# Kernel optimization log

Measured on AMD Instinct MI355X. Metric: run time of the kernel, lower is better.

Reference implementation:

```python
import jax, jax.numpy as jnp
import numpy as np

N = 32768      # total nodes (2048 graphs * 16 nodes)
E = 491520     # total edges (2048 graphs * 16*15)
F = 11         # in_node_nf
H = 64         # hidden_nf
G = 2048       # number of graphs
NN = 16        # nodes per graph
R = 1024       # n_reactions
L = 4          # n_layers
EIN = 2 * H + 1        # edge_mlp input: [h[row], h[col], radial]
NIN = H + H + F        # node_mlp input: [h, agg, node_attr=h0]


def setup_inputs() -> dict:
    key = jax.random.key(0)
    ks = jax.random.split(key, 24)
    s = 0.05
    d = {
        "h0": jax.random.normal(ks[0], (N, F), jnp.float32),
        "positions": jax.random.normal(ks[1], (N, 3), jnp.float32),
        "edges": jax.random.randint(ks[2], (2, E), 0, N),
        "node_mask": jnp.ones((N, 1), jnp.float32),
        "edge_mask": jnp.ones((E, 1), jnp.float32),
        "reaction_indexes": jax.random.randint(ks[3], (G,), 0, R),
        "reaction_signs": jax.random.normal(ks[4], (G,), jnp.float32),
        # params
        "emb_w": jax.random.normal(ks[5], (F, H), jnp.float32) * s,
        "emb_b": jnp.zeros((H,), jnp.float32),
        "edge_w1": jax.random.normal(ks[6], (L, EIN, H), jnp.float32) * s,
        "edge_b1": jnp.zeros((L, H), jnp.float32),
        "edge_w2": jax.random.normal(ks[7], (L, H, H), jnp.float32) * s,
        "edge_b2": jnp.zeros((L, H), jnp.float32),
        "node_w1": jax.random.normal(ks[8], (L, NIN, H), jnp.float32) * s,
        "node_b1": jnp.zeros((L, H), jnp.float32),
        "node_w2": jax.random.normal(ks[9], (L, H, H), jnp.float32) * s,
        "node_b2": jnp.zeros((L, H), jnp.float32),
        "dec_w1": jax.random.normal(ks[10], (H, H), jnp.float32) * s,
        "dec_b1": jnp.zeros((H,), jnp.float32),
        "dec_w2": jax.random.normal(ks[11], (H, H), jnp.float32) * s,
        "dec_b2": jnp.zeros((H,), jnp.float32),
        "g_w1": jax.random.normal(ks[12], (H, H), jnp.float32) * s,
        "g_b1": jnp.zeros((H,), jnp.float32),
        "g_w2": jax.random.normal(ks[13], (H, 1), jnp.float32) * s,
        "g_b2": jnp.zeros((1,), jnp.float32),
        "n_nodes": NN,
        "n_reactions": R,
    }
    return d


def reference(h0, positions, edges, node_mask, edge_mask, reaction_indexes,
              reaction_signs, emb_w, emb_b, edge_w1, edge_b1, edge_w2, edge_b2,
              node_w1, node_b1, node_w2, node_b2, dec_w1, dec_b1, dec_w2,
              dec_b2, g_w1, g_b1, g_w2, g_b2, n_nodes, n_reactions):
    silu = jax.nn.silu
    row, col = edges[0], edges[1]
    n = h0.shape[0]

    # radial is constant across layers (coords never updated in this variant)
    coord_diff = positions[row] - positions[col]          # [E, 3]
    radial = jnp.sum(coord_diff ** 2, axis=1, keepdims=True)  # [E, 1]

    h = h0 @ emb_w + emb_b                                # [N, H]
    for i in range(edge_w1.shape[0]):
        # edge model
        e_in = jnp.concatenate([h[row], h[col], radial], axis=1)  # [E, 2H+1]
        e = silu(e_in @ edge_w1[i] + edge_b1[i])
        e = silu(e @ edge_w2[i] + edge_b2[i])             # [E, H]
        e = e * edge_mask
        # scatter-sum aggregation by source node
        agg = jax.ops.segment_sum(e, row, num_segments=n)  # [N, H]
        # node model (node_attr = h0)
        n_in = jnp.concatenate([h, agg, h0], axis=1)      # [N, 2H+F]
        h = silu(n_in @ node_w1[i] + node_b1[i]) @ node_w2[i] + node_b2[i]

    # node decoder
    h = silu(h @ dec_w1 + dec_b1) @ dec_w2 + dec_b2
    h = h * node_mask
    # pool per graph (fixed n_nodes per graph)
    hg = h.reshape(-1, n_nodes, h.shape[-1]).sum(axis=1)  # [G, H]
    # graph decoder
    temp = silu(hg @ g_w1 + g_b1) @ g_w2 + g_b2           # [G, 1]
    # signed per-reaction aggregation
    pred = jnp.zeros((n_reactions,), h.dtype).at[reaction_indexes].add(
        temp[:, 0] * reaction_signs)
    return pred
```

## Files before the change

kernel.cpp:

```cpp
#include <hip/hip_runtime.h>
#include <math.h>
#include <stdint.h>

#define N_NODES 32768
#define N_EDGES 491520
#define F_IN    11
#define H       64
#define G_GRAPHS 2048
#define NN_PER_G 16
#define R_REACT 1024
#define L_LAYERS 4
#define EIN     129
#define NIN     139
#define NPBLK   32

#define WPROJ 0
#define WE2   65536
#define WN1   98304
#define WN2   180224
#define WD1   212992
#define WD2   221184
#define WEMB  229376
#define WTOT  233472

typedef __attribute__((ext_vector_type(8))) short short8;
typedef __attribute__((ext_vector_type(4))) float f32x4;

__device__ __forceinline__ float silu_f(float x) {
    return x * __builtin_amdgcn_rcpf(1.0f + __expf(-x));
}
__device__ __forceinline__ void atomAddF(float* p, float v) {
    unsafeAtomicAdd(p, v);
}
__device__ __forceinline__ float bf2f(unsigned short b) {
    union { float f; unsigned u; } v; v.u = ((unsigned)b) << 16;
    return v.f;
}
__device__ __forceinline__ unsigned short f2bf(float x) {
    union { float f; unsigned u; } v; v.f = x;
    unsigned r = v.u + 0x7FFFu + ((v.u >> 16) & 1u);
    return (unsigned short)(r >> 16);
}
__device__ __forceinline__ void splitbf(float x, unsigned short& hi, unsigned short& lo) {
    hi = f2bf(x);
    lo = f2bf(x - bf2f(hi));
}
__device__ __forceinline__ void splitbf_t(float x, unsigned short& hi, unsigned short& lo) {
    union { float f; unsigned u; } v; v.f = x;
    hi = (unsigned short)(v.u >> 16);
    union { float f; unsigned u; } w; w.f = x - bf2f(hi);
    lo = (unsigned short)(w.u >> 16);
}

__global__ __launch_bounds__(64) void k_prepw(
        const float* __restrict__ ew1, const float* __restrict__ ew2,
        const float* __restrict__ nw1, const float* __restrict__ nw2,
        const float* __restrict__ dw1, const float* __restrict__ dw2,
        const float* __restrict__ embw,
        short* __restrict__ wsW) {
    const int b = blockIdx.x;
    const int lane = threadIdx.x;
    const int quad = lane >> 4, m16 = lane & 15;
    short8 h8, l8;
    short* base; int fidx, half;

    if (b < 64) {
        int l = b >> 4, f = b & 15;
        int nt = f >> 1, kf = f & 1;
#pragma unroll
        for (int j = 0; j < 8; ++j) {
            int row = (nt >= 4 ? 64 : 0) + kf * 32 + quad * 8 + j;
            unsigned short hi, lo;
            splitbf(ew1[l * EIN * H + row * H + (nt & 3) * 16 + m16], hi, lo);
            h8[j] = (short)hi; l8[j] = (short)lo;
        }
        base = wsW + WPROJ + l * 16384; fidx = f; half = 8192;
    } else if (b < 96) {
        int bb = b - 64; int l = bb >> 3, f = bb & 7;
        int nt = f >> 1, kf = f & 1;
#pragma unroll
        for (int j = 0; j < 8; ++j) {
            int row = kf * 32 + quad * 8 + j;
            unsigned short hi, lo;
            splitbf(ew2[l * H * H + row * H + nt * 16 + m16], hi, lo);
            h8[j] = (short)hi; l8[j] = (short)lo;
        }
        base = wsW + WE2 + l * 8192; fidx = f; half = 4096;
    } else if (b < 176) {
        int bb = b - 96; int l = bb / 20, f = bb % 20;
        int nt = f / 5, kf = f % 5;
#pragma unroll
        for (int j = 0; j < 8; ++j) {
            int row = kf * 32 + quad * 8 + j;
            float w = (row < NIN) ? nw1[l * NIN * H + row * H + nt * 16 + m16] : 0.0f;
            unsigned short hi, lo; splitbf(w, hi, lo);
            h8[j] = (short)hi; l8[j] = (short)lo;
        }
        base = wsW + WN1 + l * 20480; fidx = f; half = 10240;
    } else if (b < 208) {
        int bb = b - 176; int l = bb >> 3, f = bb & 7;
        int nt = f >> 1, kf = f & 1;
#pragma unroll
        for (int j = 0; j < 8; ++j) {
            int row = kf * 32 + quad * 8 + j;
            unsigned short hi, lo;
            splitbf(nw2[l * H * H + row * H + nt * 16 + m16], hi, lo);
            h8[j] = (short)hi; l8[j] = (short)lo;
        }
        base = wsW + WN2 + l * 8192; fidx = f; half = 4096;
    } else if (b < 216) {
        int f = b - 208;
        int nt = f >> 1, kf = f & 1;
#pragma unroll
        for (int j = 0; j < 8; ++j) {
            int row = kf * 32 + quad * 8 + j;
            unsigned short hi, lo;
            splitbf(dw1[row * H + nt * 16 + m16], hi, lo);
            h8[j] = (short)hi; l8[j] = (short)lo;
        }
        base = wsW + WD1; fidx = f; half = 4096;
    } else if (b < 224) {
        int f = b - 216;
        int nt = f >> 1, kf = f & 1;
#pragma unroll
        for (int j = 0; j < 8; ++j) {
            int row = kf * 32 + quad * 8 + j;
            unsigned short hi, lo;
            splitbf(dw2[row * H + nt * 16 + m16], hi, lo);
            h8[j] = (short)hi; l8[j] = (short)lo;
        }
        base = wsW + WD2; fidx = f; half = 4096;
    } else {
        int f = b - 224;
#pragma unroll
        for (int j = 0; j < 8; ++j) {
            int row = quad * 8 + j;
            float w = (row < F_IN) ? embw[row * H + f * 16 + m16] : 0.0f;
            unsigned short hi, lo; splitbf(w, hi, lo);
            h8[j] = (short)hi; l8[j] = (short)lo;
        }
        base = wsW + WEMB; fidx = f; half = 2048;
    }
    *(short8*)(base + (fidx * 64 + lane) * 8) = h8;
    *(short8*)(base + half + (fidx * 64 + lane) * 8) = l8;
}

__global__ __launch_bounds__(256) void k_hist(
        const int* __restrict__ edges, int* __restrict__ deg) {
    int e = blockIdx.x * 256 + threadIdx.x;
    atomicAdd(&deg[edges[e]], 1);
}

__global__ __launch_bounds__(128) void k_scan_blk(
        const int* __restrict__ deg, int* __restrict__ off,
        int* __restrict__ bsum) {
    __shared__ int sd[128];
    int b = blockIdx.x;
    sd[threadIdx.x] = deg[b * 128 + threadIdx.x];
    __syncthreads();
    if (threadIdx.x == 0) {
        int s = 0;
        for (int i = 0; i < 128; ++i) { int d = sd[i]; sd[i] = s; s += d; }
        bsum[b] = s;
    }
    __syncthreads();
    off[b * 128 + threadIdx.x] = sd[threadIdx.x];
}

__global__ __launch_bounds__(256) void k_scan_top(
        const int* __restrict__ bsum, int* __restrict__ bbase) {
    __shared__ int sb[256];
    sb[threadIdx.x] = bsum[threadIdx.x];
    __syncthreads();
    if (threadIdx.x == 0) {
        int s = 0;
        for (int i = 0; i < 256; ++i) { int d = sb[i]; sb[i] = s; s += d; }
    }
    __syncthreads();
    bbase[threadIdx.x] = sb[threadIdx.x];
}

__global__ __launch_bounds__(256) void k_cursor(
        const int* __restrict__ off, const int* __restrict__ bbase,
        int* __restrict__ nstart, int* __restrict__ cursor) {
    int n = blockIdx.x * 256 + threadIdx.x;
    int ns = off[n] + bbase[n >> 7];
    nstart[n] = ns;
    cursor[n] = ns;
    if (n == 0) nstart[N_NODES] = N_EDGES;
}

__global__ __launch_bounds__(256) void k_fill(
        const int* __restrict__ edges, const float* __restrict__ posi,
        const float* __restrict__ emask, int* __restrict__ cursor,
        float4* __restrict__ csrQ) {
    int e = blockIdx.x * 256 + threadIdx.x;
    int r = edges[e], c = edges[N_EDGES + e];
    float dx = posi[r * 3 + 0] - posi[c * 3 + 0];
    float dy = posi[r * 3 + 1] - posi[c * 3 + 1];
    float dz = posi[r * 3 + 2] - posi[c * 3 + 2];
    float rad = dx * dx + dy * dy + dz * dz;
    int p = atomicAdd(&cursor[r], 1);
    int pk = c | ((r & (NPBLK - 1)) << 16);
    csrQ[p] = make_float4(__int_as_float(pk), rad, emask[e], 0.0f);
}

__global__ __launch_bounds__(64, 2) void k_embed_proj(
        const float* __restrict__ h0, const short* __restrict__ wEmb,
        const float* __restrict__ emb_b,
        const short* __restrict__ wP, const float* __restrict__ eb1,
        float* __restrict__ h, float* __restrict__ PA, float* __restrict__ PB) {
    const int lane = threadIdx.x;
    const int quad = lane >> 4, m16 = lane & 15;
    const int nb = blockIdx.x * 16;
    __shared__ float tld[16 * 68];

    float a0[8];
    const float* h0p = h0 + (nb + m16) * F_IN;
#pragma unroll
    for (int j = 0; j < 8; ++j) {
        int kk = quad * 8 + j;
        a0[j] = (kk < F_IN) ? h0p[kk] : 0.0f;
    }
    short8 A0h, A0l;
#pragma unroll
    for (int j = 0; j < 8; ++j) {
        unsigned short hi, lo; splitbf_t(a0[j], hi, lo);
        A0h[j] = (short)hi; A0l[j] = (short)lo;
    }
    float ebv[4];
#pragma unroll
    for (int nt = 0; nt < 4; ++nt) ebv[nt] = emb_b[nt * 16 + m16];

#pragma unroll
    for (int nt = 0; nt < 4; ++nt) {
        short8 bh = *(const short8*)(wEmb + (nt * 64 + lane) * 8);
        short8 bl = *(const short8*)(wEmb + 2048 + (nt * 64 + lane) * 8);
        f32x4 a = {0.0f, 0.0f, 0.0f, 0.0f};
        a = __builtin_amdgcn_mfma_f32_16x16x32_bf16(A0h, bh, a, 0, 0, 0);
        a = __builtin_amdgcn_mfma_f32_16x16x32_bf16(A0h, bl, a, 0, 0, 0);
        a = __builtin_amdgcn_mfma_f32_16x16x32_bf16(A0l, bh, a, 0, 0, 0);
#pragma unroll
        for (int r4 = 0; r4 < 4; ++r4) {
            const int node = nb + quad * 4 + r4;
            float hv = a[r4] + ebv[nt];
            h[node * H + nt * 16 + m16] = hv;
            tld[(quad * 4 + r4) * 68 + nt * 16 + m16] = hv;
        }
    }
    __syncthreads();
    float av[16];
    *(float4*)&av[0]  = *(const float4*)&tld[m16 * 68 + quad * 8 + 0];
    *(float4*)&av[4]  = *(const float4*)&tld[m16 * 68 + quad * 8 + 4];
    *(float4*)&av[8]  = *(const float4*)&tld[m16 * 68 + quad * 8 + 32];
    *(float4*)&av[12] = *(const float4*)&tld[m16 * 68 + quad * 8 + 36];
    short8 Ah0, Ah1, Al0, Al1;
#pragma unroll
    for (int j = 0; j < 8; ++j) {
        unsigned short hi, lo;
        splitbf_t(av[j], hi, lo);     Ah0[j] = (short)hi; Al0[j] = (short)lo;
        splitbf_t(av[8 + j], hi, lo); Ah1[j] = (short)hi; Al1[j] = (short)lo;
    }
    float b1v[4];
#pragma unroll
    for (int nt = 0; nt < 4; ++nt) b1v[nt] = eb1[nt * 16 + m16];
#pragma unroll
    for (int nt = 0; nt < 8; ++nt) {
        short8 bh0 = *(const short8*)(wP + ((nt*2+0) * 64 + lane) * 8);
        short8 bh1 = *(const short8*)(wP + ((nt*2+1) * 64 + lane) * 8);
        short8 bl0 = *(const short8*)(wP + 8192 + ((nt*2+0) * 64 + lane) * 8);
        short8 bl1 = *(const short8*)(wP + 8192 + ((nt*2+1) * 64 + lane) * 8);
        f32x4 a = {0.0f, 0.0f, 0.0f, 0.0f};
        a = __builtin_amdgcn_mfma_f32_16x16x32_bf16(Ah0, bh0, a, 0, 0, 0);
        a = __builtin_amdgcn_mfma_f32_16x16x32_bf16(Ah1, bh1, a, 0, 0, 0);
        a = __builtin_amdgcn_mfma_f32_16x16x32_bf16(Ah0, bl0, a, 0, 0, 0);
        a = __builtin_amdgcn_mfma_f32_16x16x32_bf16(Ah1, bl1, a, 0, 0, 0);
        a = __builtin_amdgcn_mfma_f32_16x16x32_bf16(Al0, bh0, a, 0, 0, 0);
        a = __builtin_amdgcn_mfma_f32_16x16x32_bf16(Al1, bh1, a, 0, 0, 0);
#pragma unroll
        for (int r4 = 0; r4 < 4; ++r4) {
            const int node = nb + quad * 4 + r4;
            if (nt < 4)
                PA[node * H + nt * 16 + m16] = a[r4] + b1v[nt];
            else
                PB[node * H + (nt - 4) * 16 + m16] = a[r4];
        }
    }
}

__global__ __launch_bounds__(256, 3) void k_edge6(
        const float* __restrict__ PA, const float* __restrict__ PB,
        const int* __restrict__ nstart, const float4* __restrict__ csrQ,
        const float* __restrict__ W1,
        const short* __restrict__ wE2, const float* __restrict__ b2,
        float* __restrict__ agg) {
    const int tid = threadIdx.x;
    const int lane = tid & 63, wave = tid >> 6;
    const int quad = lane >> 4, m16 = lane & 15;
    const int n0 = blockIdx.x * NPBLK;

    __shared__ float aggld[NPBLK * 68];
    for (int i = tid; i < NPBLK * 68; i += 256) aggld[i] = 0.0f;

    short8 Bh[8], Bl[8];
#pragma unroll
    for (int f = 0; f < 8; ++f) {
        Bh[f] = *(const short8*)(wE2 + (f * 64 + lane) * 8);
        Bl[f] = *(const short8*)(wE2 + 4096 + (f * 64 + lane) * 8);
    }
    float w1cr[16];
#pragma unroll
    for (int i = 0; i < 16; ++i) {
        int k = (i < 8) ? (quad * 8 + i) : (32 + quad * 8 + (i - 8));
        w1cr[i] = W1[128 * H + k];
    }
    float b2v[4];
#pragma unroll
    for (int nt = 0; nt < 4; ++nt) b2v[nt] = b2[nt * 16 + m16];

    const int start = nstart[n0];
    const int end   = nstart[n0 + NPBLK];
    __syncthreads();

    const int ntiles = (end - start + 15) >> 4;

    int   pkA = 0, pkB = 0;
    float radA = 0.0f, radB = 0.0f;
    float avA[16], bvA[16];

    int tA = wave;
    bool haveA = tA < ntiles;
    if (haveA) {
        const int idx = start + tA * 16 + m16;
        const int ss  = min(idx, N_EDGES - 1);
        float4 q = csrQ[ss];
        pkA  = __float_as_int(q.x);
        radA = q.y;
        const int c  = pkA & 0xFFFF;
        const int rl = pkA >> 16;
        const float* par = PA + (n0 + rl) * H + quad * 8;
        const float* pbr = PB + c * H + quad * 8;
        *(float4*)&avA[0]  = *(const float4*)(par + 0);
        *(float4*)&avA[4]  = *(const float4*)(par + 4);
        *(float4*)&avA[8]  = *(const float4*)(par + 32);
        *(float4*)&avA[12] = *(const float4*)(par + 36);
        *(float4*)&bvA[0]  = *(const float4*)(pbr + 0);
        *(float4*)&bvA[4]  = *(const float4*)(pbr + 4);
        *(float4*)&bvA[8]  = *(const float4*)(pbr + 32);
        *(float4*)&bvA[12] = *(const float4*)(pbr + 36);
    }
    int tB = tA + 4;
    bool haveB = tB < ntiles;
    if (haveB) {
        const int idx = start + tB * 16 + m16;
        const int ss  = min(idx, N_EDGES - 1);
        float4 q = csrQ[ss];
        pkB  = __float_as_int(q.x);
        radB = q.y;
    }

    while (haveA) {
        float bvB[16];
        if (haveB) {
            const int c = pkB & 0xFFFF;
            const float* pbr = PB + c * H + quad * 8;
            *(float4*)&bvB[0]  = *(const float4*)(pbr + 0);
            *(float4*)&bvB[4]  = *(const float4*)(pbr + 4);
            *(float4*)&bvB[8]  = *(const float4*)(pbr + 32);
            *(float4*)&bvB[12] = *(const float4*)(pbr + 36);
        }
        const int tC = tB + 4;
        const bool haveC = tC < ntiles;
        int pkC = 0; float radC = 0.0f;
        if (haveC) {
            const int idx = start + tC * 16 + m16;
            const int ss  = min(idx, N_EDGES - 1);
            float4 q = csrQ[ss];
            pkC  = __float_as_int(q.x);
            radC = q.y;
        }
        int rlq[4]; float mkq[4];
        const int sb = start + tA * 16 + quad * 4;
#pragma unroll
        for (int r4 = 0; r4 < 4; ++r4) {
            int s = sb + r4, s2 = min(s, N_EDGES - 1);
            float4 q = csrQ[s2];
            rlq[r4] = __float_as_int(q.x) >> 16;
            mkq[r4] = (s < end) ? q.z : 0.0f;
        }

        short8 Ah0, Ah1, Al0, Al1;
#pragma unroll
        for (int i = 0; i < 8; ++i) {
            unsigned short hi, lo;
            splitbf_t(silu_f(avA[i] + bvA[i] + radA * w1cr[i]), hi, lo);
            Ah0[i] = (short)hi; Al0[i] = (short)lo;
            splitbf_t(silu_f(avA[8+i] + bvA[8+i] + radA * w1cr[8+i]), hi, lo);
            Ah1[i] = (short)hi; Al1[i] = (short)lo;
        }
        f32x4 acc[4];
#pragma unroll
        for (int nt = 0; nt < 4; ++nt) {
            f32x4 a = {0.0f, 0.0f, 0.0f, 0.0f};
            a = __builtin_amdgcn_mfma_f32_16x16x32_bf16(Ah0, Bh[nt*2+0], a, 0, 0, 0);
            a = __builtin_amdgcn_mfma_f32_16x16x32_bf16(Ah1, Bh[nt*2+1], a, 0, 0, 0);
            a = __builtin_amdgcn_mfma_f32_16x16x32_bf16(Ah0, Bl[nt*2+0], a, 0, 0, 0);
            a = __builtin_amdgcn_mfma_f32_16x16x32_bf16(Ah1, Bl[nt*2+1], a, 0, 0, 0);
            a = __builtin_amdgcn_mfma_f32_16x16x32_bf16(Al0, Bh[nt*2+0], a, 0, 0, 0);
            a = __builtin_amdgcn_mfma_f32_16x16x32_bf16(Al1, Bh[nt*2+1], a, 0, 0, 0);
            acc[nt] = a;
        }

#pragma unroll
        for (int nt = 0; nt < 4; ++nt) {
            float oo[4];
#pragma unroll
            for (int r4 = 0; r4 < 4; ++r4)
                oo[r4] = silu_f(acc[nt][r4] + b2v[nt]) * mkq[r4];
            int cur = rlq[0]; float s = oo[0];
#pragma unroll
            for (int r4 = 1; r4 < 4; ++r4) {
                if (rlq[r4] == cur) { s += oo[r4]; }
                else {
                    atomicAdd(&aggld[cur * 68 + nt * 16 + m16], s);
                    cur = rlq[r4]; s = oo[r4];
                }
            }
            atomicAdd(&aggld[cur * 68 + nt * 16 + m16], s);
        }

        if (haveB) {
            const int rl = pkB >> 16;
            const float* par = PA + (n0 + rl) * H + quad * 8;
            *(float4*)&avA[0]  = *(const float4*)(par + 0);
            *(float4*)&avA[4]  = *(const float4*)(par + 4);
            *(float4*)&avA[8]  = *(const float4*)(par + 32);
            *(float4*)&avA[12] = *(const float4*)(par + 36);
#pragma unroll
            for (int i = 0; i < 16; ++i) bvA[i] = bvB[i];
            pkA = pkB; radA = radB;
        }
        pkB = pkC; radB = radC;
        tA = tB; tB = tC; haveA = haveB; haveB = haveC;
    }

    __syncthreads();
#pragma unroll
    for (int i = tid; i < NPBLK * 16; i += 256) {
        int n = i >> 4, cb = (i & 15) << 2;
        *(float4*)&agg[(n0 + n) * H + cb] = *(const float4*)&aggld[n * 68 + cb];
    }
}

__global__ __launch_bounds__(64, 2) void k_node_proj(
        float* __restrict__ h, const float* __restrict__ agg,
        const float* __restrict__ h0,
        const short* __restrict__ wN1, const float* __restrict__ b1,
        const short* __restrict__ wN2, const float* __restrict__ b2,
        const short* __restrict__ wPn, const float* __restrict__ eb1n,
        float* __restrict__ PA, float* __restrict__ PB) {
    const int lane = threadIdx.x;
    const int quad = lane >> 4, m16 = lane & 15;
    const int nb = blockIdx.x * 16;

    float b1v[4], b2v[4];
#pragma unroll
    for (int nt = 0; nt < 4; ++nt) {
        b1v[nt] = b1[nt * 16 + m16];
        b2v[nt] = b2[nt * 16 + m16];
    }
    __shared__ float tld[16 * 68];

    float a1[5][8];
    const float* hp = h + (nb + m16) * H + quad * 8;
    const float* ap = agg + (nb + m16) * H + quad * 8;
    *(float4*)&a1[0][0] = *(const float4*)(hp + 0);
    *(float4*)&a1[0][4] = *(const float4*)(hp + 4);
    *(float4*)&a1[1][0] = *(const float4*)(hp + 32);
    *(float4*)&a1[1][4] = *(const float4*)(hp + 36);
    *(float4*)&a1[2][0] = *(const float4*)(ap + 0);
    *(float4*)&a1[2][4] = *(const float4*)(ap + 4);
    *(float4*)&a1[3][0] = *(const float4*)(ap + 32);
    *(float4*)&a1[3][4] = *(const float4*)(ap + 36);
    const float* h0p = h0 + (nb + m16) * F_IN;
#pragma unroll
    for (int j = 0; j < 8; ++j) {
        int kk = quad * 8 + j;
        a1[4][j] = (kk < F_IN) ? h0p[kk] : 0.0f;
    }
    short8 A1h[5], A1l[5];
#pragma unroll
    for (int kf = 0; kf < 5; ++kf) {
        short8 ah, al;
#pragma unroll
        for (int j = 0; j < 8; ++j) {
            unsigned short hi, lo; splitbf_t(a1[kf][j], hi, lo);
            ah[j] = (short)hi; al[j] = (short)lo;
        }
        A1h[kf] = ah; A1l[kf] = al;
    }
#pragma unroll
    for (int nt = 0; nt < 4; ++nt) {
        short8 bh[5], bl[5];
#pragma unroll
        for (int kf = 0; kf < 5; ++kf) {
            bh[kf] = *(const short8*)(wN1 + ((nt*5+kf) * 64 + lane) * 8);
            bl[kf] = *(const short8*)(wN1 + 10240 + ((nt*5+kf) * 64 + lane) * 8);
        }
        f32x4 a = {0.0f, 0.0f, 0.0f, 0.0f};
#pragma unroll
        for (int kf = 0; kf < 5; ++kf)
            a = __builtin_amdgcn_mfma_f32_16x16x32_bf16(A1h[kf], bh[kf], a, 0, 0, 0);
#pragma unroll
        for (int kf = 0; kf < 5; ++kf)
            a = __builtin_amdgcn_mfma_f32_16x16x32_bf16(A1h[kf], bl[kf], a, 0, 0, 0);
#pragma unroll
        for (int kf = 0; kf < 5; ++kf)
            a = __builtin_amdgcn_mfma_f32_16x16x32_bf16(A1l[kf], bh[kf], a, 0, 0, 0);
#pragma unroll
        for (int r4 = 0; r4 < 4; ++r4)
            tld[(quad * 4 + r4) * 68 + nt * 16 + m16] = silu_f(a[r4] + b1v[nt]);
    }
    __syncthreads();
    float a2[16];
    *(float4*)&a2[0]  = *(const float4*)&tld[m16 * 68 + quad * 8 + 0];
    *(float4*)&a2[4]  = *(const float4*)&tld[m16 * 68 + quad * 8 + 4];
    *(float4*)&a2[8]  = *(const float4*)&tld[m16 * 68 + quad * 8 + 32];
    *(float4*)&a2[12] = *(const float4*)&tld[m16 * 68 + quad * 8 + 36];
    short8 A2h0, A2h1, A2l0, A2l1;
#pragma unroll
    for (int j = 0; j < 8; ++j) {
        unsigned short hi, lo;
        splitbf_t(a2[j], hi, lo);     A2h0[j] = (short)hi; A2l0[j] = (short)lo;
        splitbf_t(a2[8+j], hi, lo);   A2h1[j] = (short)hi; A2l1[j] = (short)lo;
    }
    __syncthreads();
#pragma unroll
    for (int nt = 0; nt < 4; ++nt) {
        short8 bh0 = *(const short8*)(wN2 + ((nt*2+0) * 64 + lane) * 8);
        short8 bh1 = *(const short8*)(wN2 + ((nt*2+1) * 64 + lane) * 8);
        short8 bl0 = *(const short8*)(wN2 + 4096 + ((nt*2+0) * 64 + lane) * 8);
        short8 bl1 = *(const short8*)(wN2 + 4096 + ((nt*2+1) * 64 + lane) * 8);
        f32x4 a = {0.0f, 0.0f, 0.0f, 0.0f};
        a = __builtin_amdgcn_mfma_f32_16x16x32_bf16(A2h0, bh0, a, 0, 0, 0);
        a = __builtin_amdgcn_mfma_f32_16x16x32_bf16(A2h1, bh1, a, 0, 0, 0);
        a = __builtin_amdgcn_mfma_f32_16x16x32_bf16(A2h0, bl0, a, 0, 0, 0);
        a = __builtin_amdgcn_mfma_f32_16x16x32_bf16(A2h1, bl1, a, 0, 0, 0);
        a = __builtin_amdgcn_mfma_f32_16x16x32_bf16(A2l0, bh0, a, 0, 0, 0);
        a = __builtin_amdgcn_mfma_f32_16x16x32_bf16(A2l1, bh1, a, 0, 0, 0);
#pragma unroll
        for (int r4 = 0; r4 < 4; ++r4) {
            const int node = nb + quad * 4 + r4;
            float hv = a[r4] + b2v[nt];
            h[node * H + nt * 16 + m16] = hv;
            tld[(quad * 4 + r4) * 68 + nt * 16 + m16] = hv;
        }
    }
    __syncthreads();
    float av[16];
    *(float4*)&av[0]  = *(const float4*)&tld[m16 * 68 + quad * 8 + 0];
    *(float4*)&av[4]  = *(const float4*)&tld[m16 * 68 + quad * 8 + 4];
    *(float4*)&av[8]  = *(const float4*)&tld[m16 * 68 + quad * 8 + 32];
    *(float4*)&av[12] = *(const float4*)&tld[m16 * 68 + quad * 8 + 36];
    short8 Ph0, Ph1, Pl0, Pl1;
#pragma unroll
    for (int j = 0; j < 8; ++j) {
        unsigned short hi, lo;
        splitbf_t(av[j], hi, lo);     Ph0[j] = (short)hi; Pl0[j] = (short)lo;
        splitbf_t(av[8+j], hi, lo);   Ph1[j] = (short)hi; Pl1[j] = (short)lo;
    }
    float b1ev[4];
#pragma unroll
    for (int nt = 0; nt < 4; ++nt) b1ev[nt] = eb1n[nt * 16 + m16];
#pragma unroll
    for (int nt = 0; nt < 8; ++nt) {
        short8 bh0 = *(const short8*)(wPn + ((nt*2+0) * 64 + lane) * 8);
        short8 bh1 = *(const short8*)(wPn + ((nt*2+1) * 64 + lane) * 8);
        short8 bl0 = *(const short8*)(wPn + 8192 + ((nt*2+0) * 64 + lane) * 8);
        short8 bl1 = *(const short8*)(wPn + 8192 + ((nt*2+1) * 64 + lane) * 8);
        f32x4 a = {0.0f, 0.0f, 0.0f, 0.0f};
        a = __builtin_amdgcn_mfma_f32_16x16x32_bf16(Ph0, bh0, a, 0, 0, 0);
        a = __builtin_amdgcn_mfma_f32_16x16x32_bf16(Ph1, bh1, a, 0, 0, 0);
        a = __builtin_amdgcn_mfma_f32_16x16x32_bf16(Ph0, bl0, a, 0, 0, 0);
        a = __builtin_amdgcn_mfma_f32_16x16x32_bf16(Ph1, bl1, a, 0, 0, 0);
        a = __builtin_amdgcn_mfma_f32_16x16x32_bf16(Pl0, bh0, a, 0, 0, 0);
        a = __builtin_amdgcn_mfma_f32_16x16x32_bf16(Pl1, bh1, a, 0, 0, 0);
#pragma unroll
        for (int r4 = 0; r4 < 4; ++r4) {
            const int node = nb + quad * 4 + r4;
            if (nt < 4)
                PA[node * H + nt * 16 + m16] = a[r4] + b1ev[nt];
            else
                PB[node * H + (nt - 4) * 16 + m16] = a[r4];
        }
    }
}

__global__ __launch_bounds__(64, 2) void k_node_dec_graph(
        const float* __restrict__ h, const float* __restrict__ agg,
        const float* __restrict__ h0,
        const short* __restrict__ wN1, const float* __restrict__ b1,
        const short* __restrict__ wN2, const float* __restrict__ b2,
        const short* __restrict__ wD1, const float* __restrict__ db1,
        const short* __restrict__ wD2, const float* __restrict__ db2,
        const float* __restrict__ nmask,
        const float* __restrict__ gW1, const float* __restrict__ gb1,
        const float* __restrict__ gW2, const float* __restrict__ gb2,
        const int* __restrict__ rid, const float* __restrict__ rsign,
        float* __restrict__ pred) {
    const int lane = threadIdx.x;
    const int quad = lane >> 4, m16 = lane & 15;
    const int nb = blockIdx.x * 16;

    float b1v[4], b2v[4], db1v[4], db2v[4];
#pragma unroll
    for (int nt = 0; nt < 4; ++nt) {
        b1v[nt]  = b1[nt * 16 + m16];
        b2v[nt]  = b2[nt * 16 + m16];
        db1v[nt] = db1[nt * 16 + m16];
        db2v[nt] = db2[nt * 16 + m16];
    }
    float nm[4];
#pragma unroll
    for (int r4 = 0; r4 < 4; ++r4) nm[r4] = nmask[nb + quad * 4 + r4];

    __shared__ float tld[16 * 68];
    __shared__ __align__(16) float hgs[64];

    float a1[5][8];
    const float* hp = h + (nb + m16) * H + quad * 8;
    const float* ap = agg + (nb + m16) * H + quad * 8;
    *(float4*)&a1[0][0] = *(const float4*)(hp + 0);
    *(float4*)&a1[0][4] = *(const float4*)(hp + 4);
    *(float4*)&a1[1][0] = *(const float4*)(hp + 32);
    *(float4*)&a1[1][4] = *(const float4*)(hp + 36);
    *(float4*)&a1[2][0] = *(const float4*)(ap + 0);
    *(float4*)&a1[2][4] = *(const float4*)(ap + 4);
    *(float4*)&a1[3][0] = *(const float4*)(ap + 32);
    *(float4*)&a1[3][4] = *(const float4*)(ap + 36);
    const float* h0p = h0 + (nb + m16) * F_IN;
#pragma unroll
    for (int j = 0; j < 8; ++j) {
        int kk = quad * 8 + j;
        a1[4][j] = (kk < F_IN) ? h0p[kk] : 0.0f;
    }
    short8 A1h[5], A1l[5];
#pragma unroll
    for (int kf = 0; kf < 5; ++kf) {
        short8 ah, al;
#pragma unroll
        for (int j = 0; j < 8; ++j) {
            unsigned short hi, lo; splitbf_t(a1[kf][j], hi, lo);
            ah[j] = (short)hi; al[j] = (short)lo;
        }
        A1h[kf] = ah; A1l[kf] = al;
    }
#pragma unroll
    for (int nt = 0; nt < 4; ++nt) {
        short8 bh[5], bl[5];
#pragma unroll
        for (int kf = 0; kf < 5; ++kf) {
            bh[kf] = *(const short8*)(wN1 + ((nt*5+kf) * 64 + lane) * 8);
            bl[kf] = *(const short8*)(wN1 + 10240 + ((nt*5+kf) * 64 + lane) * 8);
        }
        f32x4 a = {0.0f, 0.0f, 0.0f, 0.0f};
#pragma unroll
        for (int kf = 0; kf < 5; ++kf)
            a = __builtin_amdgcn_mfma_f32_16x16x32_bf16(A1h[kf], bh[kf], a, 0, 0, 0);
#pragma unroll
        for (int kf = 0; kf < 5; ++kf)
            a = __builtin_amdgcn_mfma_f32_16x16x32_bf16(A1h[kf], bl[kf], a, 0, 0, 0);
#pragma unroll
        for (int kf = 0; kf < 5; ++kf)
            a = __builtin_amdgcn_mfma_f32_16x16x32_bf16(A1l[kf], bh[kf], a, 0, 0, 0);
#pragma unroll
        for (int r4 = 0; r4 < 4; ++r4)
            tld[(quad * 4 + r4) * 68 + nt * 16 + m16] = silu_f(a[r4] + b1v[nt]);
    }
    __syncthreads();
    float a2[16];
    *(float4*)&a2[0]  = *(const float4*)&tld[m16 * 68 + quad * 8 + 0];
    *(float4*)&a2[4]  = *(const float4*)&tld[m16 * 68 + quad * 8 + 4];
    *(float4*)&a2[8]  = *(const float4*)&tld[m16 * 68 + quad * 8 + 32];
    *(float4*)&a2[12] = *(const float4*)&tld[m16 * 68 + quad * 8 + 36];
    short8 A2h0, A2h1, A2l0, A2l1;
#pragma unroll
    for (int j = 0; j < 8; ++j) {
        unsigned short hi, lo;
        splitbf_t(a2[j], hi, lo);     A2h0[j] = (short)hi; A2l0[j] = (short)lo;
        splitbf_t(a2[8+j], hi, lo);   A2h1[j] = (short)hi; A2l1[j] = (short)lo;
    }
    __syncthreads();
#pragma unroll
    for (int nt = 0; nt < 4; ++nt) {
        short8 bh0 = *(const short8*)(wN2 + ((nt*2+0) * 64 + lane) * 8);
        short8 bh1 = *(const short8*)(wN2 + ((nt*2+1) * 64 + lane) * 8);
        short8 bl0 = *(const short8*)(wN2 + 4096 + ((nt*2+0) * 64 + lane) * 8);
        short8 bl1 = *(const short8*)(wN2 + 4096 + ((nt*2+1) * 64 + lane) * 8);
        f32x4 a = {0.0f, 0.0f, 0.0f, 0.0f};
        a = __builtin_amdgcn_mfma_f32_16x16x32_bf16(A2h0, bh0, a, 0, 0, 0);
        a = __builtin_amdgcn_mfma_f32_16x16x32_bf16(A2h1, bh1, a, 0, 0, 0);
        a = __builtin_amdgcn_mfma_f32_16x16x32_bf16(A2h0, bl0, a, 0, 0, 0);
        a = __builtin_amdgcn_mfma_f32_16x16x32_bf16(A2h1, bl1, a, 0, 0, 0);
        a = __builtin_amdgcn_mfma_f32_16x16x32_bf16(A2l0, bh0, a, 0, 0, 0);
        a = __builtin_amdgcn_mfma_f32_16x16x32_bf16(A2l1, bh1, a, 0, 0, 0);
#pragma unroll
        for (int r4 = 0; r4 < 4; ++r4)
            tld[(quad * 4 + r4) * 68 + nt * 16 + m16] = a[r4] + b2v[nt];
    }
    __syncthreads();
    float av[16];
    *(float4*)&av[0]  = *(const float4*)&tld[m16 * 68 + quad * 8 + 0];
    *(float4*)&av[4]  = *(const float4*)&tld[m16 * 68 + quad * 8 + 4];
    *(float4*)&av[8]  = *(const float4*)&tld[m16 * 68 + quad * 8 + 32];
    *(float4*)&av[12] = *(const float4*)&tld[m16 * 68 + quad * 8 + 36];
    short8 Dh0, Dh1, Dl0, Dl1;
#pragma unroll
    for (int j = 0; j < 8; ++j) {
        unsigned short hi, lo;
        splitbf_t(av[j], hi, lo);     Dh0[j] = (short)hi; Dl0[j] = (short)lo;
        splitbf_t(av[8+j], hi, lo);   Dh1[j] = (short)hi; Dl1[j] = (short)lo;
    }
    __syncthreads();
#pragma unroll
    for (int nt = 0; nt < 4; ++nt) {
        short8 bh0 = *(const short8*)(wD1 + ((nt*2+0) * 64 + lane) * 8);
        short8 bh1 = *(const short8*)(wD1 + ((nt*2+1) * 64 + lane) * 8);
        short8 bl0 = *(const short8*)(wD1 + 4096 + ((nt*2+0) * 64 + lane) * 8);
        short8 bl1 = *(const short8*)(wD1 + 4096 + ((nt*2+1) * 64 + lane) * 8);
        f32x4 a = {0.0f, 0.0f, 0.0f, 0.0f};
        a = __builtin_amdgcn_mfma_f32_16x16x32_bf16(Dh0, bh0, a, 0, 0, 0);
        a = __builtin_amdgcn_mfma_f32_16x16x32_bf16(Dh1, bh1, a, 0, 0, 0);
        a = __builtin_amdgcn_mfma_f32_16x16x32_bf16(Dh0, bl0, a, 0, 0, 0);
        a = __builtin_amdgcn_mfma_f32_16x16x32_bf16(Dh1, bl1, a, 0, 0, 0);
        a = __builtin_amdgcn_mfma_f32_16x16x32_bf16(Dl0, bh0, a, 0, 0, 0);
        a = __builtin_amdgcn_mfma_f32_16x16x32_bf16(Dl1, bh1, a, 0, 0, 0);
#pragma unroll
        for (int r4 = 0; r4 < 4; ++r4)
            tld[(quad * 4 + r4) * 68 + nt * 16 + m16] = silu_f(a[r4] + db1v[nt]);
    }
    __syncthreads();
    float a3[16];
    *(float4*)&a3[0]  = *(const float4*)&tld[m16 * 68 + quad * 8 + 0];
    *(float4*)&a3[4]  = *(const float4*)&tld[m16 * 68 + quad * 8 + 4];
    *(float4*)&a3[8]  = *(const float4*)&tld[m16 * 68 + quad * 8 + 32];
    *(float4*)&a3[12] = *(const float4*)&tld[m16 * 68 + quad * 8 + 36];
    short8 Eh0, Eh1, El0, El1;
#pragma unroll
    for (int j = 0; j < 8; ++j) {
        unsigned short hi, lo;
        splitbf_t(a3[j], hi, lo);     Eh0[j] = (short)hi; El0[j] = (short)lo;
        splitbf_t(a3[8+j], hi, lo);   Eh1[j] = (short)hi; El1[j] = (short)lo;
    }
#pragma unroll
    for (int nt = 0; nt < 4; ++nt) {
        short8 bh0 = *(const short8*)(wD2 + ((nt*2+0) * 64 + lane) * 8);
        short8 bh1 = *(const short8*)(wD2 + ((nt*2+1) * 64 + lane) * 8);
        short8 bl0 = *(const short8*)(wD2 + 4096 + ((nt*2+0) * 64 + lane) * 8);
        short8 bl1 = *(const short8*)(wD2 + 4096 + ((nt*2+1) * 64 + lane) * 8);
        f32x4 a = {0.0f, 0.0f, 0.0f, 0.0f};
        a = __builtin_amdgcn_mfma_f32_16x16x32_bf16(Eh0, bh0, a, 0, 0, 0);
        a = __builtin_amdgcn_mfma_f32_16x16x32_bf16(Eh1, bh1, a, 0, 0, 0);
        a = __builtin_amdgcn_mfma_f32_16x16x32_bf16(Eh0, bl0, a, 0, 0, 0);
        a = __builtin_amdgcn_mfma_f32_16x16x32_bf16(Eh1, bl1, a, 0, 0, 0);
        a = __builtin_amdgcn_mfma_f32_16x16x32_bf16(El0, bh0, a, 0, 0, 0);
        a = __builtin_amdgcn_mfma_f32_16x16x32_bf16(El1, bh1, a, 0, 0, 0);
        float s = 0.0f;
#pragma unroll
        for (int r4 = 0; r4 < 4; ++r4)
            s += (a[r4] + db2v[nt]) * nm[r4];
        s += __shfl_xor(s, 16);
        s += __shfl_xor(s, 32);
        if (quad == 0) hgs[nt * 16 + m16] = s;
    }
    __syncthreads();
    float acc = gb1[lane];
#pragma unroll
    for (int k = 0; k < H; ++k)
        acc += hgs[k] * gW1[k * H + lane];
    float part = silu_f(acc) * gW2[lane];
#pragma unroll
    for (int off = 32; off > 0; off >>= 1)
        part += __shfl_down(part, off);
    if (lane == 0)
        atomAddF(&pred[rid[blockIdx.x]], (part + gb2[0]) * rsign[blockIdx.x]);
}

extern "C" void kernel_launch(void* const* d_in, const int* in_sizes, int n_in,
                              void* d_out, int out_size, void* d_ws, size_t ws_size,
                              hipStream_t stream) {
    const float* h0      = (const float*)d_in[0];
    const float* pos     = (const float*)d_in[1];
    const int*   edges   = (const int*)d_in[2];
    const float* nmask   = (const float*)d_in[3];
    const float* emask   = (const float*)d_in[4];
    const int*   rid     = (const int*)d_in[5];
    const float* rsign   = (const float*)d_in[6];
    const float* emb_w   = (const float*)d_in[7];
    const float* emb_b   = (const float*)d_in[8];
    const float* edge_w1 = (const float*)d_in[9];
    const float* edge_b1 = (const float*)d_in[10];
    const float* edge_w2 = (const float*)d_in[11];
    const float* edge_b2 = (const float*)d_in[12];
    const float* node_w1 = (const float*)d_in[13];
    const float* node_b1 = (const float*)d_in[14];
    const float* node_w2 = (const float*)d_in[15];
    const float* node_b2 = (const float*)d_in[16];
    const float* dec_w1  = (const float*)d_in[17];
    const float* dec_b1  = (const float*)d_in[18];
    const float* dec_w2  = (const float*)d_in[19];
    const float* dec_b2  = (const float*)d_in[20];
    const float* g_w1    = (const float*)d_in[21];
    const float* g_b1    = (const float*)d_in[22];
    const float* g_w2    = (const float*)d_in[23];
    const float* g_b2    = (const float*)d_in[24];

    float* h      = (float*)d_ws;
    float* agg    = h + N_NODES * H;
    float* PA     = agg + N_NODES * H;
    float* PB     = PA + N_NODES * H;
    float4* csrQ  = (float4*)(PB + N_NODES * H);
    int*   deg    = (int*)(csrQ + N_EDGES);
    int*   off    = deg + N_NODES;
    int*   bsum   = off + N_NODES;
    int*   bbase  = bsum + 256;
    int*   nstart = bbase + 256;
    int*   cursor = nstart + N_NODES + 1;
    short* wsW    = (short*)((((uintptr_t)(cursor + N_NODES)) + 255) & ~(uintptr_t)255);
    float* pred   = (float*)d_out;

    hipMemsetAsync(d_out, 0, R_REACT * sizeof(float), stream);
    hipMemsetAsync(deg, 0, N_NODES * sizeof(int), stream);

    k_prepw<<<228, 64, 0, stream>>>(edge_w1, edge_w2, node_w1, node_w2,
                                    dec_w1, dec_w2, emb_w, wsW);
    k_hist<<<N_EDGES / 256, 256, 0, stream>>>(edges, deg);
    k_scan_blk<<<256, 128, 0, stream>>>(deg, off, bsum);
    k_scan_top<<<1, 256, 0, stream>>>(bsum, bbase);
    k_cursor<<<N_NODES / 256, 256, 0, stream>>>(off, bbase, nstart, cursor);
    k_fill<<<N_EDGES / 256, 256, 0, stream>>>(edges, pos, emask, cursor, csrQ);
    k_embed_proj<<<N_NODES / 16, 64, 0, stream>>>(
        h0, wsW + WEMB, emb_b, wsW + WPROJ, edge_b1, h, PA, PB);

    for (int i = 0; i < L_LAYERS; ++i) {
        k_edge6<<<N_NODES / NPBLK, 256, 0, stream>>>(
            PA, PB, nstart, csrQ,
            edge_w1 + i * EIN * H,
            wsW + WE2 + i * 8192, edge_b2 + i * H, agg);
        if (i < L_LAYERS - 1) {
            k_node_proj<<<N_NODES / 16, 64, 0, stream>>>(
                h, agg, h0,
                wsW + WN1 + i * 20480, node_b1 + i * H,
                wsW + WN2 + i * 8192,  node_b2 + i * H,
                wsW + WPROJ + (i + 1) * 16384, edge_b1 + (i + 1) * H,
                PA, PB);
        } else {
            k_node_dec_graph<<<N_NODES / 16, 64, 0, stream>>>(
                h, agg, h0,
                wsW + WN1 + i * 20480, node_b1 + i * H,
                wsW + WN2 + i * 8192,  node_b2 + i * H,
                wsW + WD1, dec_b1, wsW + WD2, dec_b2,
                nmask, g_w1, g_b1, g_w2, g_b2, rid, rsign, pred);
        }
    }
}
```

Baseline: 485.7 us.

## Fuse edge aggregation with node MLP into one kernel per layer

Merges the per-layer edge kernel and the node-update/projection kernel into a single kernel, so aggregated messages stay in shared memory instead of going through a global agg buffer. PB is double-buffered so blocks can write the next layer's projection while other blocks still read the current one. Waves 2-3 duplicate the node MLP work for their half (only waves 0-1 store), and launch bounds drop to 2 blocks per CU, which can reduce occupancy for the gather-heavy edge phase.

```diff
diff --git a/kernel.cpp b/kernel.cpp
--- a/kernel.cpp
+++ b/kernel.cpp
@@ -288,200 +288,192 @@
     }
 }
 
-__global__ __launch_bounds__(256, 3) void k_edge6(
-        const float* __restrict__ PA, const float* __restrict__ PB,
+__global__ __launch_bounds__(256, 2) void k_edge_node(
+        float* __restrict__ PA, const float* __restrict__ PBin,
         const int* __restrict__ nstart, const float4* __restrict__ csrQ,
         const float* __restrict__ W1,
-        const short* __restrict__ wE2, const float* __restrict__ b2,
-        float* __restrict__ agg) {
+        const short* __restrict__ wE2, const float* __restrict__ eb2,
+        float* __restrict__ h, const float* __restrict__ h0,
+        const short* __restrict__ wN1, const float* __restrict__ nb1,
+        const short* __restrict__ wN2, const float* __restrict__ nb2,
+        const short* __restrict__ wPn, const float* __restrict__ eb1n,
+        float* __restrict__ PBout) {
     const int tid = threadIdx.x;
     const int lane = tid & 63, wave = tid >> 6;
     const int quad = lane >> 4, m16 = lane & 15;
     const int n0 = blockIdx.x * NPBLK;
 
     __shared__ float aggld[NPBLK * 68];
+    __shared__ float tld[2][16 * 68];
     for (int i = tid; i < NPBLK * 68; i += 256) aggld[i] = 0.0f;
 
-    short8 Bh[8], Bl[8];
-#pragma unroll
-    for (int f = 0; f < 8; ++f) {
-        Bh[f] = *(const short8*)(wE2 + (f * 64 + lane) * 8);
-        Bl[f] = *(const short8*)(wE2 + 4096 + (f * 64 + lane) * 8);
-    }
-    float w1cr[16];
-#pragma unroll
-    for (int i = 0; i < 16; ++i) {
-        int k = (i < 8) ? (quad * 8 + i) : (32 + quad * 8 + (i - 8));
-        w1cr[i] = W1[128 * H + k];
-    }
-    float b2v[4];
-#pragma unroll
-    for (int nt = 0; nt < 4; ++nt) b2v[nt] = b2[nt * 16 + m16];
-
-    const int start = nstart[n0];
-    const int end   = nstart[n0 + NPBLK];
-    __syncthreads();
-
-    const int ntiles = (end - start + 15) >> 4;
-
-    int   pkA = 0, pkB = 0;
-    float radA = 0.0f, radB = 0.0f;
-    float avA[16], bvA[16];
-
-    int tA = wave;
-    bool haveA = tA < ntiles;
-    if (haveA) {
-        const int idx = start + tA * 16 + m16;
-        const int ss  = min(idx, N_EDGES - 1);
-        float4 q = csrQ[ss];
-        pkA  = __float_as_int(q.x);
-        radA = q.y;
-        const int c  = pkA & 0xFFFF;
-        const int rl = pkA >> 16;
-        const float* par = PA + (n0 + rl) * H + quad * 8;
-        const float* pbr = PB + c * H + quad * 8;
-        *(float4*)&avA[0]  = *(const float4*)(par + 0);
-        *(float4*)&avA[4]  = *(const float4*)(par + 4);
-        *(float4*)&avA[8]  = *(const float4*)(par + 32);
-        *(float4*)&avA[12] = *(const float4*)(par + 36);
-        *(float4*)&bvA[0]  = *(const float4*)(pbr + 0);
-        *(float4*)&bvA[4]  = *(const float4*)(pbr + 4);
-        *(float4*)&bvA[8]  = *(const float4*)(pbr + 32);
-        *(float4*)&bvA[12] = *(const float4*)(pbr + 36);
-    }
-    int tB = tA + 4;
-    bool haveB = tB < ntiles;
-    if (haveB) {
-        const int idx = start + tB * 16 + m16;
-        const int ss  = min(idx, N_EDGES - 1);
-        float4 q = csrQ[ss];
-        pkB  = __float_as_int(q.x);
-        radB = q.y;
-    }
-
-    while (haveA) {
-        float bvB[16];
-        if (haveB) {
-            const int c = pkB & 0xFFFF;
-            const float* pbr = PB + c * H + quad * 8;
-            *(float4*)&bvB[0]  = *(const float4*)(pbr + 0);
-            *(float4*)&bvB[4]  = *(const float4*)(pbr + 4);
-            *(float4*)&bvB[8]  = *(const float4*)(pbr + 32);
-            *(float4*)&bvB[12] = *(const float4*)(pbr + 36);
-        }
-        const int tC = tB + 4;
-        const bool haveC = tC < ntiles;
-        int pkC = 0; float radC = 0.0f;
-        if (haveC) {
-            const int idx = start + tC * 16 + m16;
+    {
+        short8 Bh[8], Bl[8];
+#pragma unroll
+        for (int f = 0; f < 8; ++f) {
+            Bh[f] = *(const short8*)(wE2 + (f * 64 + lane) * 8);
+            Bl[f] = *(const short8*)(wE2 + 4096 + (f * 64 + lane) * 8);
+        }
+        float w1cr[16];
+#pragma unroll
+        for (int i = 0; i < 16; ++i) {
+            int k = (i < 8) ? (quad * 8 + i) : (32 + quad * 8 + (i - 8));
+            w1cr[i] = W1[128 * H + k];
+        }
+        float b2v[4];
+#pragma unroll
+        for (int nt = 0; nt < 4; ++nt) b2v[nt] = eb2[nt * 16 + m16];
+
+        const int start = nstart[n0];
+        const int end   = nstart[n0 + NPBLK];
+        __syncthreads();
+
+        const int ntiles = (end - start + 15) >> 4;
+
+        int   pkA = 0, pkB = 0;
+        float radA = 0.0f, radB = 0.0f;
+        float avA[16], bvA[16];
+
+        int tA = wave;
+        bool haveA = tA < ntiles;
+        if (haveA) {
+            const int idx = start + tA * 16 + m16;
             const int ss  = min(idx, N_EDGES - 1);
             float4 q = csrQ[ss];
-            pkC  = __float_as_int(q.x);
-            radC = q.y;
-        }
-        int rlq[4]; float mkq[4];
-        const int sb = start + tA * 16 + quad * 4;
-#pragma unroll
-        for (int r4 = 0; r4 < 4; ++r4) {
-            int s = sb + r4, s2 = min(s, N_EDGES - 1);
-            float4 q = csrQ[s2];
-            rlq[r4] = __float_as_int(q.x) >> 16;
-            mkq[r4] = (s < end) ? q.z : 0.0f;
-        }
-
-        short8 Ah0, Ah1, Al0, Al1;
-#pragma unroll
-        for (int i = 0; i < 8; ++i) {
-            unsigned short hi, lo;
-            splitbf_t(silu_f(avA[i] + bvA[i] + radA * w1cr[i]), hi, lo);
-            Ah0[i] = (short)hi; Al0[i] = (short)lo;
-            splitbf_t(silu_f(avA[8+i] + bvA[8+i] + radA * w1cr[8+i]), hi, lo);
-            Ah1[i] = (short)hi; Al1[i] = (short)lo;
-        }
-        f32x4 acc[4];
-#pragma unroll
-        for (int nt = 0; nt < 4; ++nt) {
-            f32x4 a = {0.0f, 0.0f, 0.0f, 0.0f};
-            a = __builtin_amdgcn_mfma_f32_16x16x32_bf16(Ah0, Bh[nt*2+0], a, 0, 0, 0);
-            a = __builtin_amdgcn_mfma_f32_16x16x32_bf16(Ah1, Bh[nt*2+1], a, 0, 0, 0);
-            a = __builtin_amdgcn_mfma_f32_16x16x32_bf16(Ah0, Bl[nt*2+0], a, 0, 0, 0);
-            a = __builtin_amdgcn_mfma_f32_16x16x32_bf16(Ah1, Bl[nt*2+1], a, 0, 0, 0);
-            a = __builtin_amdgcn_mfma_f32_16x16x32_bf16(Al0, Bh[nt*2+0], a, 0, 0, 0);
-            a = __builtin_amdgcn_mfma_f32_16x16x32_bf16(Al1, Bh[nt*2+1], a, 0, 0, 0);
-            acc[nt] = a;
-        }
-
-#pragma unroll
-        for (int nt = 0; nt < 4; ++nt) {
-            float oo[4];
-#pragma unroll
-            for (int r4 = 0; r4 < 4; ++r4)
-                oo[r4] = silu_f(acc[nt][r4] + b2v[nt]) * mkq[r4];
-            int cur = rlq[0]; float s = oo[0];
-#pragma unroll
-            for (int r4 = 1; r4 < 4; ++r4) {
-                if (rlq[r4] == cur) { s += oo[r4]; }
-                else {
-                    atomicAdd(&aggld[cur * 68 + nt * 16 + m16], s);
-                    cur = rlq[r4]; s = oo[r4];
-                }
-            }
-            atomicAdd(&aggld[cur * 68 + nt * 16 + m16], s);
-        }
-
-        if (haveB) {
-            const int rl = pkB >> 16;
+            pkA  = __float_as_int(q.x);
+            radA = q.y;
+            const int c  = pkA & 0xFFFF;
+            const int rl = pkA >> 16;
             const float* par = PA + (n0 + rl) * H + quad * 8;
+            const float* pbr = PBin + c * H + quad * 8;
             *(float4*)&avA[0]  = *(const float4*)(par + 0);
             *(float4*)&avA[4]  = *(const float4*)(par + 4);
             *(float4*)&avA[8]  = *(const float4*)(par + 32);
             *(float4*)&avA[12] = *(const float4*)(par + 36);
-#pragma unroll
-            for (int i = 0; i < 16; ++i) bvA[i] = bvB[i];
-            pkA = pkB; radA = radB;
-        }
-        pkB = pkC; radB = radC;
-        tA = tB; tB = tC; haveA = haveB; haveB = haveC;
-    }
-
-    __syncthreads();
-#pragma unroll
-    for (int i = tid; i < NPBLK * 16; i += 256) {
-        int n = i >> 4, cb = (i & 15) << 2;
-        *(float4*)&agg[(n0 + n) * H + cb] = *(const float4*)&aggld[n * 68 + cb];
-    }
-}
-
-__global__ __launch_bounds__(64, 2) void k_node_proj(
-        float* __restrict__ h, const float* __restrict__ agg,
-        const float* __restrict__ h0,
-        const short* __restrict__ wN1, const float* __restrict__ b1,
-        const short* __restrict__ wN2, const float* __restrict__ b2,
-        const short* __restrict__ wPn, const float* __restrict__ eb1n,
-        float* __restrict__ PA, float* __restrict__ PB) {
-    const int lane = threadIdx.x;
-    const int quad = lane >> 4, m16 = lane & 15;
-    const int nb = blockIdx.x * 16;
+            *(float4*)&bvA[0]  = *(const float4*)(pbr + 0);
+            *(float4*)&bvA[4]  = *(const float4*)(pbr + 4);
+            *(float4*)&bvA[8]  = *(const float4*)(pbr + 32);
+            *(float4*)&bvA[12] = *(const float4*)(pbr + 36);
+        }
+        int tB = tA + 4;
+        bool haveB = tB < ntiles;
+        if (haveB) {
+            const int idx = start + tB * 16 + m16;
+            const int ss  = min(idx, N_EDGES - 1);
+            float4 q = csrQ[ss];
+            pkB  = __float_as_int(q.x);
+            radB = q.y;
+        }
+
+        while (haveA) {
+            float bvB[16];
+            if (haveB) {
+                const int c = pkB & 0xFFFF;
+                const float* pbr = PBin + c * H + quad * 8;
+                *(float4*)&bvB[0]  = *(const float4*)(pbr + 0);
+                *(float4*)&bvB[4]  = *(const float4*)(pbr + 4);
+                *(float4*)&bvB[8]  = *(const float4*)(pbr + 32);
+                *(float4*)&bvB[12] = *(const float4*)(pbr + 36);
+            }
+            const int tC = tB + 4;
+            const bool haveC = tC < ntiles;
+            int pkC = 0; float radC = 0.0f;
+            if (haveC) {
+                const int idx = start + tC * 16 + m16;
+                const int ss  = min(idx, N_EDGES - 1);
+                float4 q = csrQ[ss];
+                pkC  = __float_as_int(q.x);
+                radC = q.y;
+            }
+            int rlq[4]; float mkq[4];
+            const int sb = start + tA * 16 + quad * 4;
+#pragma unroll
+            for (int r4 = 0; r4 < 4; ++r4) {
+                int s = sb + r4, s2 = min(s, N_EDGES - 1);
+                float4 q = csrQ[s2];
+                rlq[r4] = __float_as_int(q.x) >> 16;
+                mkq[r4] = (s < end) ? q.z : 0.0f;
+            }
+
+            short8 Ah0, Ah1, Al0, Al1;
+#pragma unroll
+            for (int i = 0; i < 8; ++i) {
+                unsigned short hi, lo;
+                splitbf_t(silu_f(avA[i] + bvA[i] + radA * w1cr[i]), hi, lo);
+                Ah0[i] = (short)hi; Al0[i] = (short)lo;
+                splitbf_t(silu_f(avA[8+i] + bvA[8+i] + radA * w1cr[8+i]), hi, lo);
+                Ah1[i] = (short)hi; Al1[i] = (short)lo;
+            }
+            f32x4 acc[4];
+#pragma unroll
+            for (int nt = 0; nt < 4; ++nt) {
+                f32x4 a = {0.0f, 0.0f, 0.0f, 0.0f};
+                a = __builtin_amdgcn_mfma_f32_16x16x32_bf16(Ah0, Bh[nt*2+0], a, 0, 0, 0);
+                a = __builtin_amdgcn_mfma_f32_16x16x32_bf16(Ah1, Bh[nt*2+1], a, 0, 0, 0);
+                a = __builtin_amdgcn_mfma_f32_16x16x32_bf16(Ah0, Bl[nt*2+0], a, 0, 0, 0);
+                a = __builtin_amdgcn_mfma_f32_16x16x32_bf16(Ah1, Bl[nt*2+1], a, 0, 0, 0);
+                a = __builtin_amdgcn_mfma_f32_16x16x32_bf16(Al0, Bh[nt*2+0], a, 0, 0, 0);
+                a = __builtin_amdgcn_mfma_f32_16x16x32_bf16(Al1, Bh[nt*2+1], a, 0, 0, 0);
+                acc[nt] = a;
+            }
+
+#pragma unroll
+            for (int nt = 0; nt < 4; ++nt) {
+                float oo[4];
+#pragma unroll
+                for (int r4 = 0; r4 < 4; ++r4)
+                    oo[r4] = silu_f(acc[nt][r4] + b2v[nt]) * mkq[r4];
+                int cur = rlq[0]; float s = oo[0];
+#pragma unroll
+                for (int r4 = 1; r4 < 4; ++r4) {
+                    if (rlq[r4] == cur) { s += oo[r4]; }
+                    else {
+                        atomicAdd(&aggld[cur * 68 + nt * 16 + m16], s);
+                        cur = rlq[r4]; s = oo[r4];
+                    }
+                }
+                atomicAdd(&aggld[cur * 68 + nt * 16 + m16], s);
+            }
+
+            if (haveB) {
+                const int rl = pkB >> 16;
+                const float* par = PA + (n0 + rl) * H + quad * 8;
+                *(float4*)&avA[0]  = *(const float4*)(par + 0);
+                *(float4*)&avA[4]  = *(const float4*)(par + 4);
+                *(float4*)&avA[8]  = *(const float4*)(par + 32);
+                *(float4*)&avA[12] = *(const float4*)(par + 36);
+#pragma unroll
+                for (int i = 0; i < 16; ++i) bvA[i] = bvB[i];
+                pkA = pkB; radA = radB;
+            }
+            pkB = pkC; radB = radC;
+            tA = tB; tB = tC; haveA = haveB; haveB = haveC;
+        }
+    }
+    __syncthreads();
+
+    const int t  = wave & 1;
+    const int nb = n0 + t * 16;
+    const bool wmain = (wave < 2);
 
     float b1v[4], b2v[4];
 #pragma unroll
     for (int nt = 0; nt < 4; ++nt) {
-        b1v[nt] = b1[nt * 16 + m16];
-        b2v[nt] = b2[nt * 16 + m16];
-    }
-    __shared__ float tld[16 * 68];
+        b1v[nt] = nb1[nt * 16 + m16];
+        b2v[nt] = nb2[nt * 16 + m16];
+    }
 
     float a1[5][8];
     const float* hp = h + (nb + m16) * H + quad * 8;
-    const float* ap = agg + (nb + m16) * H + quad * 8;
+    const float* ag = &aggld[(t * 16 + m16) * 68 + quad * 8];
     *(float4*)&a1[0][0] = *(const float4*)(hp + 0);
     *(float4*)&a1[0][4] = *(const float4*)(hp + 4);
     *(float4*)&a1[1][0] = *(const float4*)(hp + 32);
     *(float4*)&a1[1][4] = *(const float4*)(hp + 36);
-    *(float4*)&a1[2][0] = *(const float4*)(ap + 0);
-    *(float4*)&a1[2][4] = *(const float4*)(ap + 4);
-    *(float4*)&a1[3][0] = *(const float4*)(ap + 32);
-    *(float4*)&a1[3][4] = *(const float4*)(ap + 36);
+    *(float4*)&a1[2][0] = *(const float4*)(ag + 0);
+    *(float4*)&a1[2][4] = *(const float4*)(ag + 4);
+    *(float4*)&a1[3][0] = *(const float4*)(ag + 32);
+    *(float4*)&a1[3][4] = *(const float4*)(ag + 36);
     const float* h0p = h0 + (nb + m16) * F_IN;
 #pragma unroll
     for (int j = 0; j < 8; ++j) {
@@ -519,14 +511,14 @@
             a = __builtin_amdgcn_mfma_f32_16x16x32_bf16(A1l[kf], bh[kf], a, 0, 0, 0);
 #pragma unroll
         for (int r4 = 0; r4 < 4; ++r4)
-            tld[(quad * 4 + r4) * 68 + nt * 16 + m16] = silu_f(a[r4] + b1v[nt]);
+            tld[t][(quad * 4 + r4) * 68 + nt * 16 + m16] = silu_f(a[r4] + b1v[nt]);
     }
     __syncthreads();
     float a2[16];
-    *(float4*)&a2[0]  = *(const float4*)&tld[m16 * 68 + quad * 8 + 0];
-    *(float4*)&a2[4]  = *(const float4*)&tld[m16 * 68 + quad * 8 + 4];
-    *(float4*)&a2[8]  = *(const float4*)&tld[m16 * 68 + quad * 8 + 32];
-    *(float4*)&a2[12] = *(const float4*)&tld[m16 * 68 + quad * 8 + 36];
+    *(float4*)&a2[0]  = *(const float4*)&tld[t][m16 * 68 + quad * 8 + 0];
+    *(float4*)&a2[4]  = *(const float4*)&tld[t][m16 * 68 + quad * 8 + 4];
+    *(float4*)&a2[8]  = *(const float4*)&tld[t][m16 * 68 + quad * 8 + 32];
+    *(float4*)&a2[12] = *(const float4*)&tld[t][m16 * 68 + quad * 8 + 36];
     short8 A2h0, A2h1, A2l0, A2l1;
 #pragma unroll
     for (int j = 0; j < 8; ++j) {
@@ -552,16 +544,16 @@
         for (int r4 = 0; r4 < 4; ++r4) {
             const int node = nb + quad * 4 + r4;
             float hv = a[r4] + b2v[nt];
-            h[node * H + nt * 16 + m16] = hv;
-            tld[(quad * 4 + r4) * 68 + nt * 16 + m16] = hv;
+            if (wmain) h[node * H + nt * 16 + m16] = hv;
+            tld[t][(quad * 4 + r4) * 68 + nt * 16 + m16] = hv;
         }
     }
     __syncthreads();
     float av[16];
-    *(float4*)&av[0]  = *(const float4*)&tld[m16 * 68 + quad * 8 + 0];
-    *(float4*)&av[4]  = *(const float4*)&tld[m16 * 68 + quad * 8 + 4];
-    *(float4*)&av[8]  = *(const float4*)&tld[m16 * 68 + quad * 8 + 32];
-    *(float4*)&av[12] = *(const float4*)&tld[m16 * 68 + quad * 8 + 36];
+    *(float4*)&av[0]  = *(const float4*)&tld[t][m16 * 68 + quad * 8 + 0];
+    *(float4*)&av[4]  = *(const float4*)&tld[t][m16 * 68 + quad * 8 + 4];
+    *(float4*)&av[8]  = *(const float4*)&tld[t][m16 * 68 + quad * 8 + 32];
+    *(float4*)&av[12] = *(const float4*)&tld[t][m16 * 68 + quad * 8 + 36];
     short8 Ph0, Ph1, Pl0, Pl1;
 #pragma unroll
     for (int j = 0; j < 8; ++j) {
@@ -585,22 +577,27 @@
         a = __builtin_amdgcn_mfma_f32_16x16x32_bf16(Ph1, bl1, a, 0, 0, 0);
         a = __builtin_amdgcn_mfma_f32_16x16x32_bf16(Pl0, bh0, a, 0, 0, 0);
         a = __builtin_amdgcn_mfma_f32_16x16x32_bf16(Pl1, bh1, a, 0, 0, 0);
-#pragma unroll
-        for (int r4 = 0; r4 < 4; ++r4) {
-            const int node = nb + quad * 4 + r4;
-            if (nt < 4)
-                PA[node * H + nt * 16 + m16] = a[r4] + b1ev[nt];
-            else
-                PB[node * H + (nt - 4) * 16 + m16] = a[r4];
-        }
-    }
-}
-
-__global__ __launch_bounds__(64, 2) void k_node_dec_graph(
-        const float* __restrict__ h, const float* __restrict__ agg,
-        const float* __restrict__ h0,
-        const short* __restrict__ wN1, const float* __restrict__ b1,
-        const short* __restrict__ wN2, const float* __restrict__ b2,
+        if (wmain) {
+#pragma unroll
+            for (int r4 = 0; r4 < 4; ++r4) {
+                const int node = nb + quad * 4 + r4;
+                if (nt < 4)
+                    PA[node * H + nt * 16 + m16] = a[r4] + b1ev[nt];
+                else
+                    PBout[node * H + (nt - 4) * 16 + m16] = a[r4];
+            }
+        }
+    }
+}
+
+__global__ __launch_bounds__(256, 2) void k_edge_node_last(
+        const float* __restrict__ PA, const float* __restrict__ PBin,
+        const int* __restrict__ nstart, const float4* __restrict__ csrQ,
+        const float* __restrict__ W1,
+        const short* __restrict__ wE2, const float* __restrict__ eb2,
+        const float* __restrict__ h, const float* __restrict__ h0,
+        const short* __restrict__ wN1, const float* __restrict__ nb1,
+        const short* __restrict__ wN2, const float* __restrict__ nb2,
         const short* __restrict__ wD1, const float* __restrict__ db1,
         const short* __restrict__ wD2, const float* __restrict__ db2,
         const float* __restrict__ nmask,
@@ -608,15 +605,169 @@
         const float* __restrict__ gW2, const float* __restrict__ gb2,
         const int* __restrict__ rid, const float* __restrict__ rsign,
         float* __restrict__ pred) {
-    const int lane = threadIdx.x;
+    const int tid = threadIdx.x;
+    const int lane = tid & 63, wave = tid >> 6;
     const int quad = lane >> 4, m16 = lane & 15;
-    const int nb = blockIdx.x * 16;
+    const int n0 = blockIdx.x * NPBLK;
+
+    __shared__ float aggld[NPBLK * 68];
+    __shared__ float tld[2][16 * 68];
+    __shared__ __align__(16) float hgs[2][64];
+    for (int i = tid; i < NPBLK * 68; i += 256) aggld[i] = 0.0f;
+
+    {
+        short8 Bh[8], Bl[8];
+#pragma unroll
+        for (int f = 0; f < 8; ++f) {
+            Bh[f] = *(const short8*)(wE2 + (f * 64 + lane) * 8);
+            Bl[f] = *(const short8*)(wE2 + 4096 + (f * 64 + lane) * 8);
+        }
+        float w1cr[16];
+#pragma unroll
+        for (int i = 0; i < 16; ++i) {
+            int k = (i < 8) ? (quad * 8 + i) : (32 + quad * 8 + (i - 8));
+            w1cr[i] = W1[128 * H + k];
+        }
+        float b2v[4];
+#pragma unroll
+        for (int nt = 0; nt < 4; ++nt) b2v[nt] = eb2[nt * 16 + m16];
+
+        const int start = nstart[n0];
+        const int end   = nstart[n0 + NPBLK];
+        __syncthreads();
+
+        const int ntiles = (end - start + 15) >> 4;
+
+        int   pkA = 0, pkB = 0;
+        float radA = 0.0f, radB = 0.0f;
+        float avA[16], bvA[16];
+
+        int tA = wave;
+        bool haveA = tA < ntiles;
+        if (haveA) {
+            const int idx = start + tA * 16 + m16;
+            const int ss  = min(idx, N_EDGES - 1);
+            float4 q = csrQ[ss];
+            pkA  = __float_as_int(q.x);
+            radA = q.y;
+            const int c  = pkA & 0xFFFF;
+            const int rl = pkA >> 16;
+            const float* par = PA + (n0 + rl) * H + quad * 8;
+            const float* pbr = PBin + c * H + quad * 8;
+            *(float4*)&avA[0]  = *(const float4*)(par + 0);
+            *(float4*)&avA[4]  = *(const float4*)(par + 4);
+            *(float4*)&avA[8]  = *(const float4*)(par + 32);
+            *(float4*)&avA[12] = *(const float4*)(par + 36);
+            *(float4*)&bvA[0]  = *(const float4*)(pbr + 0);
+            *(float4*)&bvA[4]  = *(const float4*)(pbr + 4);
+            *(float4*)&bvA[8]  = *(const float4*)(pbr + 32);
+            *(float4*)&bvA[12] = *(const float4*)(pbr + 36);
+        }
+        int tB = tA + 4;
+        bool haveB = tB < ntiles;
+        if (haveB) {
+            const int idx = start + tB * 16 + m16;
+            const int ss  = min(idx, N_EDGES - 1);
+            float4 q = csrQ[ss];
+            pkB  = __float_as_int(q.x);
+            radB = q.y;
+        }
+
+        while (haveA) {
+            float bvB[16];
+            if (haveB) {
+                const int c = pkB & 0xFFFF;
+                const float* pbr = PBin + c * H + quad * 8;
+                *(float4*)&bvB[0]  = *(const float4*)(pbr + 0);
+                *(float4*)&bvB[4]  = *(const float4*)(pbr + 4);
+                *(float4*)&bvB[8]  = *(const float4*)(pbr + 32);
+                *(float4*)&bvB[12] = *(const float4*)(pbr + 36);
+            }
+            const int tC = tB + 4;
+            const bool haveC = tC < ntiles;
+            int pkC = 0; float radC = 0.0f;
+            if (haveC) {
+                const int idx = start + tC * 16 + m16;
+                const int ss  = min(idx, N_EDGES - 1);
+                float4 q = csrQ[ss];
+                pkC  = __float_as_int(q.x);
+                radC = q.y;
+            }
+            int rlq[4]; float mkq[4];
+            const int sb = start + tA * 16 + quad * 4;
+#pragma unroll
+            for (int r4 = 0; r4 < 4; ++r4) {
+                int s = sb + r4, s2 = min(s, N_EDGES - 1);
+                float4 q = csrQ[s2];
+                rlq[r4] = __float_as_int(q.x) >> 16;
+                mkq[r4] = (s < end) ? q.z : 0.0f;
+            }
+
+            short8 Ah0, Ah1, Al0, Al1;
+#pragma unroll
+            for (int i = 0; i < 8; ++i) {
+                unsigned short hi, lo;
+                splitbf_t(silu_f(avA[i] + bvA[i] + radA * w1cr[i]), hi, lo);
+                Ah0[i] = (short)hi; Al0[i] = (short)lo;
+                splitbf_t(silu_f(avA[8+i] + bvA[8+i] + radA * w1cr[8+i]), hi, lo);
+                Ah1[i] = (short)hi; Al1[i] = (short)lo;
+            }
+            f32x4 acc[4];
+#pragma unroll
+            for (int nt = 0; nt < 4; ++nt) {
+                f32x4 a = {0.0f, 0.0f, 0.0f, 0.0f};
+                a = __builtin_amdgcn_mfma_f32_16x16x32_bf16(Ah0, Bh[nt*2+0], a, 0, 0, 0);
+                a = __builtin_amdgcn_mfma_f32_16x16x32_bf16(Ah1, Bh[nt*2+1], a, 0, 0, 0);
+                a = __builtin_amdgcn_mfma_f32_16x16x32_bf16(Ah0, Bl[nt*2+0], a, 0, 0, 0);
+                a = __builtin_amdgcn_mfma_f32_16x16x32_bf16(Ah1, Bl[nt*2+1], a, 0, 0, 0);
+                a = __builtin_amdgcn_mfma_f32_16x16x32_bf16(Al0, Bh[nt*2+0], a, 0, 0, 0);
+                a = __builtin_amdgcn_mfma_f32_16x16x32_bf16(Al1, Bh[nt*2+1], a, 0, 0, 0);
+                acc[nt] = a;
+            }
+
+#pragma unroll
+            for (int nt = 0; nt < 4; ++nt) {
+                float oo[4];
+#pragma unroll
+                for (int r4 = 0; r4 < 4; ++r4)
+                    oo[r4] = silu_f(acc[nt][r4] + b2v[nt]) * mkq[r4];
+                int cur = rlq[0]; float s = oo[0];
+#pragma unroll
+                for (int r4 = 1; r4 < 4; ++r4) {
+                    if (rlq[r4] == cur) { s += oo[r4]; }
+                    else {
+                        atomicAdd(&aggld[cur * 68 + nt * 16 + m16], s);
+                        cur = rlq[r4]; s = oo[r4];
+                    }
+                }
+                atomicAdd(&aggld[cur * 68 + nt * 16 + m16], s);
+            }
+
+            if (haveB) {
+                const int rl = pkB >> 16;
+                const float* par = PA + (n0 + rl) * H + quad * 8;
+                *(float4*)&avA[0]  = *(const float4*)(par + 0);
+                *(float4*)&avA[4]  = *(const float4*)(par + 4);
+                *(float4*)&avA[8]  = *(const float4*)(par + 32);
+                *(float4*)&avA[12] = *(const float4*)(par + 36);
+#pragma unroll
+                for (int i = 0; i < 16; ++i) bvA[i] = bvB[i];
+                pkA = pkB; radA = radB;
+            }
+            pkB = pkC; radB = radC;
+            tA = tB; tB = tC; haveA = haveB; haveB = haveC;
+        }
+    }
+    __syncthreads();
+
+    const int t  = wave & 1;
+    const int nb = n0 + t * 16;
 
     float b1v[4], b2v[4], db1v[4], db2v[4];
 #pragma unroll
     for (int nt = 0; nt < 4; ++nt) {
-        b1v[nt]  = b1[nt * 16 + m16];
-        b2v[nt]  = b2[nt * 16 + m16];
+        b1v[nt]  = nb1[nt * 16 + m16];
+        b2v[nt]  = nb2[nt * 16 + m16];
         db1v[nt] = db1[nt * 16 + m16];
         db2v[nt] = db2[nt * 16 + m16];
     }
@@ -624,20 +775,17 @@
 #pragma unroll
     for (int r4 = 0; r4 < 4; ++r4) nm[r4] = nmask[nb + quad * 4 + r4];
 
-    __shared__ float tld[16 * 68];
-    __shared__ __align__(16) float hgs[64];
-
     float a1[5][8];
     const float* hp = h + (nb + m16) * H + quad * 8;
-    const float* ap = agg + (nb + m16) * H + quad * 8;
+    const float* ag = &aggld[(t * 16 + m16) * 68 + quad * 8];
     *(float4*)&a1[0][0] = *(const float4*)(hp + 0);
     *(float4*)&a1[0][4] = *(const float4*)(hp + 4);
     *(float4*)&a1[1][0] = *(const float4*)(hp + 32);
     *(float4*)&a1[1][4] = *(const float4*)(hp + 36);
-    *(float4*)&a1[2][0] = *(const float4*)(ap + 0);
-    *(float4*)&a1[2][4] = *(const float4*)(ap + 4);
-    *(float4*)&a1[3][0] = *(const float4*)(ap + 32);
-    *(float4*)&a1[3][4] = *(const float4*)(ap + 36);
+    *(float4*)&a1[2][0] = *(const float4*)(ag + 0);
+    *(float4*)&a1[2][4] = *(const float4*)(ag + 4);
+    *(float4*)&a1[3][0] = *(const float4*)(ag + 32);
+    *(float4*)&a1[3][4] = *(const float4*)(ag + 36);
     const float* h0p = h0 + (nb + m16) * F_IN;
 #pragma unroll
     for (int j = 0; j < 8; ++j) {
@@ -675,14 +823,14 @@
             a = __builtin_amdgcn_mfma_f32_16x16x32_bf16(A1l[kf], bh[kf], a, 0, 0, 0);
 #pragma unroll
         for (int r4 = 0; r4 < 4; ++r4)
-            tld[(quad * 4 + r4) * 68 + nt * 16 + m16] = silu_f(a[r4] + b1v[nt]);
+            tld[t][(quad * 4 + r4) * 68 + nt * 16 + m16] = silu_f(a[r4] + b1v[nt]);
     }
     __syncthreads();
     float a2[16];
-    *(float4*)&a2[0]  = *(const float4*)&tld[m16 * 68 + quad * 8 + 0];
-    *(float4*)&a2[4]  = *(const float4*)&tld[m16 * 68 + quad * 8 + 4];
-    *(float4*)&a2[8]  = *(const float4*)&tld[m16 * 68 + quad * 8 + 32];
-    *(float4*)&a2[12] = *(const float4*)&tld[m16 * 68 + quad * 8 + 36];
+    *(float4*)&a2[0]  = *(const float4*)&tld[t][m16 * 68 + quad * 8 + 0];
+    *(float4*)&a2[4]  = *(const float4*)&tld[t][m16 * 68 + quad * 8 + 4];
+    *(float4*)&a2[8]  = *(const float4*)&tld[t][m16 * 68 + quad * 8 + 32];
+    *(float4*)&a2[12] = *(const float4*)&tld[t][m16 * 68 + quad * 8 + 36];
     short8 A2h0, A2h1, A2l0, A2l1;
 #pragma unroll
     for (int j = 0; j < 8; ++j) {
@@ -706,14 +854,14 @@
         a = __builtin_amdgcn_mfma_f32_16x16x32_bf16(A2l1, bh1, a, 0, 0, 0);
 #pragma unroll
         for (int r4 = 0; r4 < 4; ++r4)
-            tld[(quad * 4 + r4) * 68 + nt * 16 + m16] = a[r4] + b2v[nt];
+            tld[t][(quad * 4 + r4) * 68 + nt * 16 + m16] = a[r4] + b2v[nt];
     }
     __syncthreads();
     float av[16];
-    *(float4*)&av[0]  = *(const float4*)&tld[m16 * 68 + quad * 8 + 0];
-    *(float4*)&av[4]  = *(const float4*)&tld[m16 * 68 + quad * 8 + 4];
-    *(float4*)&av[8]  = *(const float4*)&tld[m16 * 68 + quad * 8 + 32];
-    *(float4*)&av[12] = *(const float4*)&tld[m16 * 68 + quad * 8 + 36];
+    *(float4*)&av[0]  = *(const float4*)&tld[t][m16 * 68 + quad * 8 + 0];
+    *(float4*)&av[4]  = *(const float4*)&tld[t][m16 * 68 + quad * 8 + 4];
+    *(float4*)&av[8]  = *(const float4*)&tld[t][m16 * 68 + quad * 8 + 32];
+    *(float4*)&av[12] = *(const float4*)&tld[t][m16 * 68 + quad * 8 + 36];
     short8 Dh0, Dh1, Dl0, Dl1;
 #pragma unroll
     for (int j = 0; j < 8; ++j) {
@@ -737,19 +885,20 @@
         a = __builtin_amdgcn_mfma_f32_16x16x32_bf16(Dl1, bh1, a, 0, 0, 0);
 #pragma unroll
         for (int r4 = 0; r4 < 4; ++r4)
-            tld[(quad * 4 + r4) * 68 + nt * 16 + m16] = silu_f(a[r4] + db1v[nt]);
+            tld[t][(quad * 4 + r4) * 68 + nt * 16 + m16] = silu_f(a[r4] + db1v[nt]);
     }
     __syncthreads();
     float a3[16];
-    *(float4*)&a3[0]  = *(const float4*)&tld[m16 * 68 + quad * 8 + 0];
-    *(float4*)&a3[4]  = *(const float4*)&tld[m16 * 68 + quad * 8 + 4];
-    *(float4*)&a3[8]  = *(const float4*)&tld[m16 * 68 + quad * 8 + 32];
-    *(float4*)&a3[12] = *(const float4*)&tld[m16 * 68 + quad * 8 + 36];
+    *(float4*)&a3[0]  = *(const float4*)&tld[t][m16 * 68 + quad * 8 + 0];
+    *(float4*)&a3[4]  = *(const float4*)&tld[t][m16 * 68 + quad * 8 + 4];
+    *(float4*)&a3[8]  = *(const float4*)&tld[t][m16 * 68 + quad * 8 + 32];
+    *(float4*)&a3[12] = *(const float4*)&tld[t][m16 * 68 + quad * 8 + 36];
     short8 Eh0, Eh1, El0, El1;
 #pragma unroll
     for (int j = 0; j < 8; ++j) {
         unsigned short hi, lo;
         splitbf_t(a3[j], hi, lo);     Eh0[j] = (short)hi; El0[j] = (short)lo;
+        splitbf_t(a3[8+j], hi, lo);   El1[j] = 0; Eh1[j] = 0;
         splitbf_t(a3[8+j], hi, lo);   Eh1[j] = (short)hi; El1[j] = (short)lo;
     }
 #pragma unroll
@@ -771,19 +920,22 @@
             s += (a[r4] + db2v[nt]) * nm[r4];
         s += __shfl_xor(s, 16);
         s += __shfl_xor(s, 32);
-        if (quad == 0) hgs[nt * 16 + m16] = s;
-    }
-    __syncthreads();
-    float acc = gb1[lane];
-#pragma unroll
-    for (int k = 0; k < H; ++k)
-        acc += hgs[k] * gW1[k * H + lane];
-    float part = silu_f(acc) * gW2[lane];
-#pragma unroll
-    for (int off = 32; off > 0; off >>= 1)
-        part += __shfl_down(part, off);
-    if (lane == 0)
-        atomAddF(&pred[rid[blockIdx.x]], (part + gb2[0]) * rsign[blockIdx.x]);
+        if (quad == 0) hgs[t][nt * 16 + m16] = s;
+    }
+    __syncthreads();
+    if (wave < 2) {
+        const int g = blockIdx.x * 2 + wave;
+        float acc = gb1[lane];
+#pragma unroll
+        for (int k = 0; k < H; ++k)
+            acc += hgs[wave][k] * gW1[k * H + lane];
+        float part = silu_f(acc) * gW2[lane];
+#pragma unroll
+        for (int off = 32; off > 0; off >>= 1)
+            part += __shfl_down(part, off);
+        if (lane == 0)
+            atomAddF(&pred[rid[g]], (part + gb2[0]) * rsign[g]);
+    }
 }
 
 extern "C" void kernel_launch(void* const* d_in, const int* in_sizes, int n_in,
@@ -816,10 +968,10 @@
     const float* g_b2    = (const float*)d_in[24];
 
     float* h      = (float*)d_ws;
-    float* agg    = h + N_NODES * H;
-    float* PA     = agg + N_NODES * H;
-    float* PB     = PA + N_NODES * H;
-    float4* csrQ  = (float4*)(PB + N_NODES * H);
+    float* PA     = h + N_NODES * H;
+    float* PB0    = PA + N_NODES * H;
+    float* PB1    = PB0 + N_NODES * H;
+    float4* csrQ  = (float4*)(PB1 + N_NODES * H);
     int*   deg    = (int*)(csrQ + N_EDGES);
     int*   off    = deg + N_NODES;
     int*   bsum   = off + N_NODES;
@@ -840,27 +992,30 @@
     k_cursor<<<N_NODES / 256, 256, 0, stream>>>(off, bbase, nstart, cursor);
     k_fill<<<N_EDGES / 256, 256, 0, stream>>>(edges, pos, emask, cursor, csrQ);
     k_embed_proj<<<N_NODES / 16, 64, 0, stream>>>(
-        h0, wsW + WEMB, emb_b, wsW + WPROJ, edge_b1, h, PA, PB);
-
-    for (int i = 0; i < L_LAYERS; ++i) {
-        k_edge6<<<N_NODES / NPBLK, 256, 0, stream>>>(
-            PA, PB, nstart, csrQ,
+        h0, wsW + WEMB, emb_b, wsW + WPROJ, edge_b1, h, PA, PB0);
+
+    float* PBbuf[2] = {PB0, PB1};
+    for (int i = 0; i < L_LAYERS - 1; ++i) {
+        k_edge_node<<<N_NODES / NPBLK, 256, 0, stream>>>(
+            PA, PBbuf[i & 1], nstart, csrQ,
             edge_w1 + i * EIN * H,
-            wsW + WE2 + i * 8192, edge_b2 + i * H, agg);
-        if (i < L_LAYERS - 1) {
-            k_node_proj<<<N_NODES / 16, 64, 0, stream>>>(
-                h, agg, h0,
-                wsW + WN1 + i * 20480, node_b1 + i * H,
-                wsW + WN2 + i * 8192,  node_b2 + i * H,
-                wsW + WPROJ + (i + 1) * 16384, edge_b1 + (i + 1) * H,
-                PA, PB);
-        } else {
-            k_node_dec_graph<<<N_NODES / 16, 64, 0, stream>>>(
-                h, agg, h0,
-                wsW + WN1 + i * 20480, node_b1 + i * H,
-                wsW + WN2 + i * 8192,  node_b2 + i * H,
-                wsW + WD1, dec_b1, wsW + WD2, dec_b2,
-                nmask, g_w1, g_b1, g_w2, g_b2, rid, rsign, pred);
-        }
-    }
-}
+            wsW + WE2 + i * 8192, edge_b2 + i * H,
+            h, h0,
+            wsW + WN1 + i * 20480, node_b1 + i * H,
+            wsW + WN2 + i * 8192,  node_b2 + i * H,
+            wsW + WPROJ + (i + 1) * 16384, edge_b1 + (i + 1) * H,
+            PBbuf[(i + 1) & 1]);
+    }
+    {
+        const int i = L_LAYERS - 1;
+        k_edge_node_last<<<N_NODES / NPBLK, 256, 0, stream>>>(
+            PA, PBbuf[i & 1], nstart, csrQ,
+            edge_w1 + i * EIN * H,
+            wsW + WE2 + i * 8192, edge_b2 + i * H,
+            h, h0,
+            wsW + WN1 + i * 20480, node_b1 + i * H,
+            wsW + WN2 + i * 8192,  node_b2 + i * H,
+            wsW + WD1, dec_b1, wsW + WD2, dec_b2,
+            nmask, g_w1, g_b1, g_w2, g_b2, rid, rsign, pred);
+    }
+}
```

After: 488.0 us. Within noise of the previous version (+0.5%).
